# Kernel tuning notes

Measured on AMD Instinct MI355X. Metric: run time of the kernel, lower is better.

The kernel has to match this reference:

```python
import jax, jax.numpy as jnp
import numpy as np

N = 100000      # nodes
E = 1600000     # edges (avg degree 16)
D_IN = 128
D_H = 128
D_OUT = 64


def setup_inputs() -> dict:
    key = jax.random.key(0)
    k1, k2, k3, k4, k5 = jax.random.split(key, 5)
    x = jax.random.normal(k1, (N, D_IN), dtype=jnp.float32)
    edge_row = jax.random.randint(k2, (E,), 0, N, dtype=jnp.int32)
    # guarantee every destination row has at least one neighbor (no div-by-zero)
    edge_row = edge_row.at[:N].set(jnp.arange(N, dtype=jnp.int32))
    edge_col = jax.random.randint(k3, (E,), 0, N, dtype=jnp.int32)
    # xavier_uniform init as in the torch module
    lim1 = float(np.sqrt(6.0 / (D_IN + D_H)))
    W1 = jax.random.uniform(k4, (D_IN, D_H), jnp.float32, -lim1, lim1)
    lim2 = float(np.sqrt(6.0 / (D_H + D_OUT)))
    W2 = jax.random.uniform(k5, (D_H, D_OUT), jnp.float32, -lim2, lim2)
    return {"x": x, "W1": W1, "W2": W2, "edge_row": edge_row, "edge_col": edge_col}


def _mean_aggregate(h, edge_row, edge_col):
    # spmm(adjacency, h) with binary COO adjacency: out[i] = sum_{(i,j) in E} h[j]
    support = jax.ops.segment_sum(h[edge_col], edge_row, num_segments=N)  # [N, d]
    num_neigh = jax.ops.segment_sum(
        jnp.ones((edge_row.shape[0],), dtype=h.dtype), edge_row, num_segments=N
    )  # [N] = adjacency.sum(dim=1)
    return support / num_neigh[:, None]


def reference(x, W1, W2, edge_row, edge_col):
    # layer 1: GraphSAGEConv + relu
    h = jax.nn.relu(_mean_aggregate(x @ W1, edge_row, edge_col))
    # layer 2 (last): GraphSAGEConv, no activation -> logits
    logits = _mean_aggregate(h @ W2, edge_row, edge_col)
    return logits
```

## Files before the change

### kernel.cpp

```cpp
#include <hip/hip_runtime.h>


#define DIN 128
#define DH 128
#define DOUT 64

#define BSH 9
#define COLB 17
#define COLM ((1 << COLB) - 1)
#define LRM ((1 << BSH) - 1)
#define CHUNK 4096
#define CH_PT 16

typedef __attribute__((ext_vector_type(8))) short short8;
typedef __attribute__((ext_vector_type(4))) float floatx4;

__device__ __forceinline__ unsigned bfpack(float a, float b) {
    unsigned ua = __float_as_uint(a);
    unsigned ub = __float_as_uint(b);
    ua += 0x7fffu + ((ua >> 16) & 1u);
    ub += 0x7fffu + ((ub >> 16) & 1u);
    return (ua >> 16) | (ub & 0xffff0000u);
}
__device__ __forceinline__ unsigned short bf1(float a) {
    unsigned u = __float_as_uint(a);
    u += 0x7fffu + ((u >> 16) & 1u);
    return (unsigned short)(u >> 16);
}

__global__ __launch_bounds__(256) void k_prep(const float* __restrict__ W1,
                                              const float* __restrict__ W2,
                                              unsigned short* __restrict__ Wt1,
                                              unsigned short* __restrict__ Wt2) {
    int idx = blockIdx.x * 256 + threadIdx.x;
    if (idx < 128 * 128) {
        int k = idx >> 7, nn = idx & 127;
        Wt1[nn * 128 + k] = bf1(W1[idx]);
    }
    int i2 = idx - 128 * 128;
    if (i2 >= 0 && i2 < 128 * 64) {
        int k = i2 >> 6, nn = i2 & 63;
        Wt2[nn * 128 + k] = bf1(W2[i2]);
    }
}


__global__ __launch_bounds__(256) void k_hist(const int* __restrict__ row,
                                              int* __restrict__ HT,
                                              int E, int nb, int nch) {
    __shared__ int h[512];
    int t = threadIdx.x, c = blockIdx.x;
    for (int i = t; i < nb; i += 256) h[i] = 0;
    __syncthreads();
    int base = c * CHUNK;
#pragma unroll
    for (int i = 0; i < CH_PT; ++i) {
        int e = base + i * 256 + t;
        if (e < E) atomicAdd(&h[row[e] >> BSH], 1);
    }
    __syncthreads();
    for (int i = t; i < nb; i += 256) HT[(size_t)i * nch + c] = h[i];
}

__global__ __launch_bounds__(256) void k_hscan_row(int* __restrict__ HT,
                                                   int* __restrict__ bsum,
                                                   int nch) {
    __shared__ int sh[256];
    int b = blockIdx.x, t = threadIdx.x;
    int carry = 0;
    for (int tile = 0; tile < nch; tile += 256) {
        int idx = tile + t;
        int v = (idx < nch) ? HT[(size_t)b * nch + idx] : 0;
        sh[t] = v;
        __syncthreads();
        for (int d = 1; d < 256; d <<= 1) {
            int u = (t >= d) ? sh[t - d] : 0;
            __syncthreads();
            sh[t] += u;
            __syncthreads();
        }
        if (idx < nch) HT[(size_t)b * nch + idx] = carry + sh[t] - v;
        carry += sh[255];
        __syncthreads();
    }
    if (t == 0) bsum[b] = carry;
}

__global__ __launch_bounds__(256) void k_hscan_base(const int* __restrict__ bsum,
                                                    int* __restrict__ bucketBase,
                                                    int nb, int E) {
    __shared__ int sh[256];
    int t = threadIdx.x;
    int v = (t < nb) ? bsum[t] : 0;
    sh[t] = v;
    __syncthreads();
    for (int d = 1; d < 256; d <<= 1) {
        int u = (t >= d) ? sh[t - d] : 0;
        __syncthreads();
        sh[t] += u;
        __syncthreads();
    }
    if (t < nb) bucketBase[t] = sh[t] - v;
    if (t == 0) bucketBase[nb] = E;
}

__global__ __launch_bounds__(256) void k_part(const int* __restrict__ row,
                                              const int* __restrict__ col,
                                              const int* __restrict__ HT,
                                              const int* __restrict__ bucketBase,
                                              int* __restrict__ packed,
                                              int E, int nb, int nch) {
    __shared__ int cur[512];
    int t = threadIdx.x, c = blockIdx.x;
    for (int i = t; i < nb; i += 256)
        cur[i] = HT[(size_t)i * nch + c] + bucketBase[i];
    __syncthreads();
    int base = c * CHUNK;
#pragma unroll
    for (int i = 0; i < CH_PT; ++i) {
        int e = base + i * 256 + t;
        if (e < E) {
            int r = row[e], cc = col[e];
            int b = r >> BSH;
            int pos = atomicAdd(&cur[b], 1);
            packed[pos] = ((r & LRM) << COLB) | cc;
        }
    }
}

__global__ __launch_bounds__(256) void k_build(const int* __restrict__ packed,
                                               const int* __restrict__ bucketBase,
                                               int* __restrict__ csr,
                                               int* __restrict__ offs,
                                               int* __restrict__ degc,
                                               float* __restrict__ invdeg,
                                               int N, int nb) {
    __shared__ int hist[512], scn[512], part[256];
    int t = threadIdx.x, b = blockIdx.x;
    int lo = bucketBase[b], hi = bucketBase[b + 1];
    int base_row = b << BSH;
    int nloc = N - base_row; if (nloc > 512) nloc = 512;
    hist[t] = 0; hist[t + 256] = 0;
    __syncthreads();
    for (int e = lo + t; e < hi; e += 256)
        atomicAdd(&hist[packed[e] >> COLB], 1);
    __syncthreads();
    int a = hist[2 * t], b2 = hist[2 * t + 1];
    part[t] = a + b2;
    __syncthreads();
    for (int d = 1; d < 256; d <<= 1) {
        int v = (t >= d) ? part[t - d] : 0;
        __syncthreads();
        part[t] += v;
        __syncthreads();
    }
    int bp = (t == 0) ? 0 : part[t - 1];
    scn[2 * t] = bp;
    scn[2 * t + 1] = bp + a;
    __syncthreads();
    for (int i = t; i < nloc; i += 256) {
        int r = base_row + i;
        offs[r] = lo + scn[i];
        int d = hist[i];
        degc[r] = d;
        invdeg[r] = 1.0f / (float)d;
    }
    __syncthreads();
    for (int e = lo + t; e < hi; e += 256) {
        int p = packed[e];
        int pos = lo + atomicAdd(&scn[p >> COLB], 1);
        csr[pos] = p & COLM;
    }
}


__global__ __launch_bounds__(256) void k_gemm1(const float* __restrict__ X,
                                               const unsigned short* __restrict__ Wt,
                                               unsigned short* __restrict__ H1b, int n) {
    __shared__ unsigned short xs[64][136];
    __shared__ unsigned short wt[128][136];
    int tid = threadIdx.x;
    int r0 = blockIdx.x * 64;

    for (int i = tid; i < 64 * 32; i += 256) {
        int r = i >> 5, c4 = i & 31;
        float4 v = make_float4(0.f, 0.f, 0.f, 0.f);
        if (r0 + r < n) v = ((const float4*)X)[(size_t)(r0 + r) * 32 + c4];
        *(uint2*)&xs[r][c4 * 4] = make_uint2(bfpack(v.x, v.y), bfpack(v.z, v.w));
    }
    for (int i = tid; i < 128 * 16; i += 256) {
        int r = i >> 4, c = i & 15;
        *(uint4*)&wt[r][c * 8] = ((const uint4*)Wt)[r * 16 + c];
    }
    __syncthreads();

    int w = tid >> 6, lane = tid & 63;
    int ml = lane & 15, q = lane >> 4;
    floatx4 acc[8];
#pragma unroll
    for (int t = 0; t < 8; ++t) acc[t] = (floatx4)(0.f);

#pragma unroll
    for (int kc = 0; kc < 4; ++kc) {
        short8 af = *(const short8*)&xs[w * 16 + ml][kc * 32 + q * 8];
#pragma unroll
        for (int nt = 0; nt < 8; ++nt) {
            short8 bf = *(const short8*)&wt[nt * 16 + ml][kc * 32 + q * 8];
            acc[nt] = __builtin_amdgcn_mfma_f32_16x16x32_bf16(af, bf, acc[nt], 0, 0, 0);
        }
    }
#pragma unroll
    for (int nt = 0; nt < 8; ++nt)
#pragma unroll
        for (int r = 0; r < 4; ++r) {
            int rr = r0 + w * 16 + q * 4 + r;
            if (rr < n)
                H1b[(size_t)rr * 128 + nt * 16 + ml] = bf1(acc[nt][r]);
        }
}

__global__ __launch_bounds__(256) void k_gemm2(const unsigned* __restrict__ Hin,
                                               const unsigned short* __restrict__ Wt,
                                               unsigned short* __restrict__ H2b, int n) {
    __shared__ unsigned short xs[64][136];
    __shared__ unsigned short wt[64][136];
    int tid = threadIdx.x;
    int r0 = blockIdx.x * 64;

    for (int i = tid; i < 64 * 16; i += 256) {
        int r = i >> 4, c = i & 15;
        uint4 v = make_uint4(0u, 0u, 0u, 0u);
        if (r0 + r < n) v = ((const uint4*)Hin)[(size_t)(r0 + r) * 16 + c];
        *(uint4*)&xs[r][c * 8] = v;
    }
    for (int i = tid; i < 64 * 16; i += 256) {
        int r = i >> 4, c = i & 15;
        *(uint4*)&wt[r][c * 8] = ((const uint4*)Wt)[r * 16 + c];
    }
    __syncthreads();

    int w = tid >> 6, lane = tid & 63;
    int ml = lane & 15, q = lane >> 4;
    floatx4 acc[4];
#pragma unroll
    for (int t = 0; t < 4; ++t) acc[t] = (floatx4)(0.f);

#pragma unroll
    for (int kc = 0; kc < 4; ++kc) {
        short8 af = *(const short8*)&xs[w * 16 + ml][kc * 32 + q * 8];
#pragma unroll
        for (int nt = 0; nt < 4; ++nt) {
            short8 bf = *(const short8*)&wt[nt * 16 + ml][kc * 32 + q * 8];
            acc[nt] = __builtin_amdgcn_mfma_f32_16x16x32_bf16(af, bf, acc[nt], 0, 0, 0);
        }
    }
#pragma unroll
    for (int nt = 0; nt < 4; ++nt)
#pragma unroll
        for (int r = 0; r < 4; ++r) {
            int rr = r0 + w * 16 + q * 4 + r;
            if (rr < n)
                H2b[(size_t)rr * 64 + nt * 16 + ml] = bf1(acc[nt][r]);
        }
}


__global__ __launch_bounds__(256) void k_agg1(const unsigned* __restrict__ H1b,
                                              const int* __restrict__ offs,
                                              const int* __restrict__ degc,
                                              const float* __restrict__ invdeg,
                                              const int* __restrict__ csr,
                                              unsigned* __restrict__ Hout, int n) {
    int wave = threadIdx.x >> 6, lane = threadIdx.x & 63;
    int row = blockIdx.x * 4 + wave;
    if (row >= n) return;
    int start = offs[row], d = degc[row];
    float s0[8], s1[8];
#pragma unroll
    for (int j = 0; j < 8; ++j) { s0[j] = 0.f; s1[j] = 0.f; }
    int i = 0;
    for (; i + 8 <= d; i += 8) {
        int idx[8];
#pragma unroll
        for (int j = 0; j < 8; ++j) idx[j] = csr[start + i + j];
        unsigned v[8];
#pragma unroll
        for (int j = 0; j < 8; ++j) v[j] = H1b[(size_t)idx[j] * 64 + lane];
#pragma unroll
        for (int j = 0; j < 8; ++j) {
            s0[j] += __uint_as_float(v[j] << 16);
            s1[j] += __uint_as_float(v[j] & 0xffff0000u);
        }
    }
    for (; i < d; ++i) {
        int c = csr[start + i];
        unsigned v = H1b[(size_t)c * 64 + lane];
        s0[0] += __uint_as_float(v << 16);
        s1[0] += __uint_as_float(v & 0xffff0000u);
    }
    float t0 = (s0[0] + s0[1]) + (s0[2] + s0[3]) + ((s0[4] + s0[5]) + (s0[6] + s0[7]));
    float t1 = (s1[0] + s1[1]) + (s1[2] + s1[3]) + ((s1[4] + s1[5]) + (s1[6] + s1[7]));
    float inv = invdeg[row];
    t0 = fmaxf(t0 * inv, 0.f);
    t1 = fmaxf(t1 * inv, 0.f);
    Hout[(size_t)row * 64 + lane] = bfpack(t0, t1);
}

__global__ __launch_bounds__(256) void k_agg2(const unsigned short* __restrict__ H2b,
                                              const int* __restrict__ offs,
                                              const int* __restrict__ degc,
                                              const float* __restrict__ invdeg,
                                              const int* __restrict__ csr,
                                              float* __restrict__ Out, int n) {
    int wave = threadIdx.x >> 6, lane = threadIdx.x & 63;
    int row = blockIdx.x * 4 + wave;
    if (row >= n) return;
    int start = offs[row], d = degc[row];
    float s[8];
#pragma unroll
    for (int j = 0; j < 8; ++j) s[j] = 0.f;
    int i = 0;
    for (; i + 8 <= d; i += 8) {
        int idx[8];
#pragma unroll
        for (int j = 0; j < 8; ++j) idx[j] = csr[start + i + j];
        unsigned short v[8];
#pragma unroll
        for (int j = 0; j < 8; ++j) v[j] = H2b[(size_t)idx[j] * 64 + lane];
#pragma unroll
        for (int j = 0; j < 8; ++j)
            s[j] += __uint_as_float(((unsigned)v[j]) << 16);
    }
    for (; i < d; ++i) {
        int c = csr[start + i];
        s[0] += __uint_as_float(((unsigned)H2b[(size_t)c * 64 + lane]) << 16);
    }
    float t = (s[0] + s[1]) + (s[2] + s[3]) + ((s[4] + s[5]) + (s[6] + s[7]));
    Out[(size_t)row * 64 + lane] = t * invdeg[row];
}

extern "C" void kernel_launch(void* const* d_in, const int* in_sizes, int n_in,
                              void* d_out, int out_size, void* d_ws, size_t ws_size,
                              hipStream_t stream) {
    const float* x    = (const float*)d_in[0];
    const float* W1   = (const float*)d_in[1];
    const float* W2   = (const float*)d_in[2];
    const int*   erow = (const int*)d_in[3];
    const int*   ecol = (const int*)d_in[4];
    const int N = in_sizes[0] / DIN;
    const int E = in_sizes[3];

    const int nb  = (N + (1 << BSH) - 1) >> BSH;
    const int nch = (E + CHUNK - 1) / CHUNK;

    size_t o = 0;
    auto take = [&](size_t nbytes) {
        void* p = (char*)d_ws + o;
        o += (nbytes + 255) & ~(size_t)255;
        return p;
    };
    int*            HT     = (int*)take((size_t)nb * nch * 4);
    int*            bsum   = (int*)take((size_t)nb * 4);
    int*            bbase  = (int*)take((size_t)(nb + 1) * 4);
    int*            packed = (int*)take((size_t)E * 4);
    int*            csr    = (int*)take((size_t)E * 4);
    int*            offs   = (int*)take((size_t)N * 4);
    int*            degc   = (int*)take((size_t)N * 4);
    float*          invdeg = (float*)take((size_t)N * 4);
    unsigned short* Wt1    = (unsigned short*)take(128 * 128 * 2);
    unsigned short* Wt2    = (unsigned short*)take(64 * 128 * 2);
    unsigned*       h1b    = (unsigned*)take((size_t)N * DH * 2);
    unsigned*       h      = (unsigned*)take((size_t)N * DH * 2);
    unsigned*       h2b    = h1b;

    k_prep      <<<96,  256, 0, stream>>>(W1, W2, Wt1, Wt2);
    k_hist      <<<nch, 256, 0, stream>>>(erow, HT, E, nb, nch);
    k_hscan_row <<<nb,  256, 0, stream>>>(HT, bsum, nch);
    k_hscan_base<<<1,   256, 0, stream>>>(bsum, bbase, nb, E);
    k_part      <<<nch, 256, 0, stream>>>(erow, ecol, HT, bbase, packed, E, nb, nch);
    k_build     <<<nb,  256, 0, stream>>>(packed, bbase, csr, offs, degc, invdeg, N, nb);
    k_gemm1<<<(N + 63) / 64, 256, 0, stream>>>(x, Wt1, (unsigned short*)h1b, N);
    k_agg1 <<<(N + 3) / 4, 256, 0, stream>>>(h1b, offs, degc, invdeg, csr, h, N);
    k_gemm2<<<(N + 63) / 64, 256, 0, stream>>>(h, Wt2, (unsigned short*)h2b, N);
    k_agg2 <<<(N + 3) / 4, 256, 0, stream>>>((const unsigned short*)h2b, offs, degc,
                                             invdeg, csr, (float*)d_out, N);
}
```

Baseline: 310.3 us.

## Use 16-byte vector gathers with multi-edge-per-wave lane groups in aggregation

```diff
diff --git a/kernel.cpp b/kernel.cpp
--- a/kernel.cpp
+++ b/kernel.cpp
@@ -26,6 +26,17 @@
     unsigned u = __float_as_uint(a);
     u += 0x7fffu + ((u >> 16) & 1u);
     return (unsigned short)(u >> 16);
+}
+
+__device__ __forceinline__ void acc8(float* a, uint4 v) {
+    a[0] += __uint_as_float(v.x << 16);
+    a[1] += __uint_as_float(v.x & 0xffff0000u);
+    a[2] += __uint_as_float(v.y << 16);
+    a[3] += __uint_as_float(v.y & 0xffff0000u);
+    a[4] += __uint_as_float(v.z << 16);
+    a[5] += __uint_as_float(v.z & 0xffff0000u);
+    a[6] += __uint_as_float(v.w << 16);
+    a[7] += __uint_as_float(v.w & 0xffff0000u);
 }
 
 __global__ __launch_bounds__(256) void k_prep(const float* __restrict__ W1,
@@ -265,48 +276,62 @@
 }
 
 
-__global__ __launch_bounds__(256) void k_agg1(const unsigned* __restrict__ H1b,
+__global__ __launch_bounds__(256) void k_agg1(const uint4* __restrict__ H1b,
                                               const int* __restrict__ offs,
                                               const int* __restrict__ degc,
                                               const float* __restrict__ invdeg,
                                               const int* __restrict__ csr,
-                                              unsigned* __restrict__ Hout, int n) {
+                                              uint4* __restrict__ Hout, int n) {
     int wave = threadIdx.x >> 6, lane = threadIdx.x & 63;
     int row = blockIdx.x * 4 + wave;
     if (row >= n) return;
     int start = offs[row], d = degc[row];
-    float s0[8], s1[8];
-#pragma unroll
-    for (int j = 0; j < 8; ++j) { s0[j] = 0.f; s1[j] = 0.f; }
+    int g = lane >> 4;
+    int sl = lane & 15;
+
+    float acc[8];
+#pragma unroll
+    for (int k = 0; k < 8; ++k) acc[k] = 0.f;
+
     int i = 0;
     for (; i + 8 <= d; i += 8) {
-        int idx[8];
-#pragma unroll
-        for (int j = 0; j < 8; ++j) idx[j] = csr[start + i + j];
-        unsigned v[8];
-#pragma unroll
-        for (int j = 0; j < 8; ++j) v[j] = H1b[(size_t)idx[j] * 64 + lane];
-#pragma unroll
-        for (int j = 0; j < 8; ++j) {
-            s0[j] += __uint_as_float(v[j] << 16);
-            s1[j] += __uint_as_float(v[j] & 0xffff0000u);
-        }
-    }
-    for (; i < d; ++i) {
-        int c = csr[start + i];
-        unsigned v = H1b[(size_t)c * 64 + lane];
-        s0[0] += __uint_as_float(v << 16);
-        s1[0] += __uint_as_float(v & 0xffff0000u);
-    }
-    float t0 = (s0[0] + s0[1]) + (s0[2] + s0[3]) + ((s0[4] + s0[5]) + (s0[6] + s0[7]));
-    float t1 = (s1[0] + s1[1]) + (s1[2] + s1[3]) + ((s1[4] + s1[5]) + (s1[6] + s1[7]));
-    float inv = invdeg[row];
-    t0 = fmaxf(t0 * inv, 0.f);
-    t1 = fmaxf(t1 * inv, 0.f);
-    Hout[(size_t)row * 64 + lane] = bfpack(t0, t1);
-}
-
-__global__ __launch_bounds__(256) void k_agg2(const unsigned short* __restrict__ H2b,
+        int c0 = csr[start + i + g];
+        int c1 = csr[start + i + 4 + g];
+        uint4 v0 = H1b[((unsigned)c0 << 4) + sl];
+        uint4 v1 = H1b[((unsigned)c1 << 4) + sl];
+        acc8(acc, v0);
+        acc8(acc, v1);
+    }
+    for (; i < d; i += 4) {
+        int j = i + g;
+        uint4 v = make_uint4(0u, 0u, 0u, 0u);
+        if (j < d) {
+            int c = csr[start + j];
+            v = H1b[((unsigned)c << 4) + sl];
+        }
+        acc8(acc, v);
+    }
+
+#pragma unroll
+    for (int k = 0; k < 8; ++k) {
+        acc[k] += __shfl_xor(acc[k], 16);
+        acc[k] += __shfl_xor(acc[k], 32);
+    }
+
+    if (g == 0) {
+        float inv = invdeg[row];
+#pragma unroll
+        for (int k = 0; k < 8; ++k) acc[k] = fmaxf(acc[k] * inv, 0.f);
+        uint4 o;
+        o.x = bfpack(acc[0], acc[1]);
+        o.y = bfpack(acc[2], acc[3]);
+        o.z = bfpack(acc[4], acc[5]);
+        o.w = bfpack(acc[6], acc[7]);
+        Hout[(size_t)row * 16 + sl] = o;
+    }
+}
+
+__global__ __launch_bounds__(256) void k_agg2(const uint4* __restrict__ H2b,
                                               const int* __restrict__ offs,
                                               const int* __restrict__ degc,
                                               const float* __restrict__ invdeg,
@@ -316,27 +341,49 @@
     int row = blockIdx.x * 4 + wave;
     if (row >= n) return;
     int start = offs[row], d = degc[row];
-    float s[8];
-#pragma unroll
-    for (int j = 0; j < 8; ++j) s[j] = 0.f;
+    int g = lane >> 3;
+    int sl = lane & 7;
+
+    float acc[8];
+#pragma unroll
+    for (int k = 0; k < 8; ++k) acc[k] = 0.f;
+
     int i = 0;
-    for (; i + 8 <= d; i += 8) {
-        int idx[8];
-#pragma unroll
-        for (int j = 0; j < 8; ++j) idx[j] = csr[start + i + j];
-        unsigned short v[8];
-#pragma unroll
-        for (int j = 0; j < 8; ++j) v[j] = H2b[(size_t)idx[j] * 64 + lane];
-#pragma unroll
-        for (int j = 0; j < 8; ++j)
-            s[j] += __uint_as_float(((unsigned)v[j]) << 16);
-    }
-    for (; i < d; ++i) {
-        int c = csr[start + i];
-        s[0] += __uint_as_float(((unsigned)H2b[(size_t)c * 64 + lane]) << 16);
-    }
-    float t = (s[0] + s[1]) + (s[2] + s[3]) + ((s[4] + s[5]) + (s[6] + s[7]));
-    Out[(size_t)row * 64 + lane] = t * invdeg[row];
+    for (; i + 16 <= d; i += 16) {
+        int c0 = csr[start + i + g];
+        int c1 = csr[start + i + 8 + g];
+        uint4 v0 = H2b[((unsigned)c0 << 3) + sl];
+        uint4 v1 = H2b[((unsigned)c1 << 3) + sl];
+        acc8(acc, v0);
+        acc8(acc, v1);
+    }
+    for (; i < d; i += 8) {
+        int j = i + g;
+        uint4 v = make_uint4(0u, 0u, 0u, 0u);
+        if (j < d) {
+            int c = csr[start + j];
+            v = H2b[((unsigned)c << 3) + sl];
+        }
+        acc8(acc, v);
+    }
+
+#pragma unroll
+    for (int k = 0; k < 8; ++k) {
+        acc[k] += __shfl_xor(acc[k], 8);
+        acc[k] += __shfl_xor(acc[k], 16);
+        acc[k] += __shfl_xor(acc[k], 32);
+    }
+
+    if (g == 0) {
+        float inv = invdeg[row];
+        float4 o0, o1;
+        o0.x = acc[0] * inv; o0.y = acc[1] * inv;
+        o0.z = acc[2] * inv; o0.w = acc[3] * inv;
+        o1.x = acc[4] * inv; o1.y = acc[5] * inv;
+        o1.z = acc[6] * inv; o1.w = acc[7] * inv;
+        ((float4*)Out)[(size_t)row * 16 + sl * 2]     = o0;
+        ((float4*)Out)[(size_t)row * 16 + sl * 2 + 1] = o1;
+    }
 }
 
 extern "C" void kernel_launch(void* const* d_in, const int* in_sizes, int n_in,
@@ -380,8 +427,9 @@
     k_part      <<<nch, 256, 0, stream>>>(erow, ecol, HT, bbase, packed, E, nb, nch);
     k_build     <<<nb,  256, 0, stream>>>(packed, bbase, csr, offs, degc, invdeg, N, nb);
     k_gemm1<<<(N + 63) / 64, 256, 0, stream>>>(x, Wt1, (unsigned short*)h1b, N);
-    k_agg1 <<<(N + 3) / 4, 256, 0, stream>>>(h1b, offs, degc, invdeg, csr, h, N);
+    k_agg1 <<<(N + 3) / 4, 256, 0, stream>>>((const uint4*)h1b, offs, degc, invdeg,
+                                             csr, (uint4*)h, N);
     k_gemm2<<<(N + 63) / 64, 256, 0, stream>>>(h, Wt2, (unsigned short*)h2b, N);
-    k_agg2 <<<(N + 3) / 4, 256, 0, stream>>>((const unsigned short*)h2b, offs, degc,
+    k_agg2 <<<(N + 3) / 4, 256, 0, stream>>>((const uint4*)h2b, offs, degc,
                                              invdeg, csr, (float*)d_out, N);
 }
```

After: 274.3 us. 11.6% less time.
